# Performance work log

Hardware: AMD Instinct MI355X
Metric: run time of the kernel (lower is better)

The kernel has to match this reference:

```python
import jax, jax.numpy as jnp
import numpy as np

KERNEL = 3          # kernel_size = (3, 3)
DEGREE = 3          # spline_order -> Chebyshev polynomial degree
N_CONVS = 8


def setup_inputs() -> dict:
    key = jax.random.key(0)
    k1, k2, k3, k4 = jax.random.split(key, 4)
    x = jax.random.normal(k1, (16, 16, 128, 128), jnp.float32)
    # per-conv learned params of ChebyshevKANLinear(in=9, out=1), stacked over n_convs
    cheby_coeffs = jax.random.normal(k2, (N_CONVS, KERNEL * KERNEL, DEGREE + 1), jnp.float32) * 0.1
    base_weight = jax.random.normal(k3, (N_CONVS, KERNEL * KERNEL), jnp.float32) * (1.0 / 3.0)
    spline_scaler = 1.0 + 0.1 * jax.random.normal(k4, (N_CONVS, KERNEL * KERNEL), jnp.float32)
    return {"x": x, "cheby_coeffs": cheby_coeffs,
            "base_weight": base_weight, "spline_scaler": spline_scaler}


def _kan_conv2d(x, cheby_coeffs, base_weight, spline_scaler):
    # x: (B, C, H, W); each channel unfolded independently (as torch Unfold per-channel),
    # each of N_CONVS KAN kernels applied to every channel -> out channels C*N_CONVS.
    B, C, H, W = x.shape
    patches = jax.lax.conv_general_dilated_patches(
        x, (KERNEL, KERNEL), (1, 1), [(1, 1), (1, 1)])  # (B, C*9, Ho, Wo), channel-major
    Ho, Wo = patches.shape[-2], patches.shape[-1]
    p = patches.reshape(B, C, KERNEL * KERNEL, Ho * Wo)
    p = jnp.moveaxis(p, 2, 3)  # (B, C, P, 9) where P = Ho*Wo patches

    # base (skip) path: SiLU(x) @ base_weight^T
    base = jnp.einsum('bcpi,ji->bcjp', jax.nn.silu(p), base_weight)

    # spline path: Chebyshev basis on tanh-normalized input
    t = jnp.tanh(p)
    Ts = [jnp.ones_like(t), t]
    for _ in range(DEGREE - 1):
        Ts.append(2.0 * t * Ts[-1] - Ts[-2])
    Tb = jnp.stack(Ts, axis=-1)  # (B, C, P, 9, DEGREE+1)
    w = cheby_coeffs * spline_scaler[..., None]  # (n_convs, 9, D+1)
    spline = jnp.einsum('bcpik,jik->bcjp', Tb, w)

    out = (base + spline).reshape(B, C * N_CONVS, Ho, Wo)
    return out


def reference(x, cheby_coeffs, base_weight, spline_scaler):
    return _kan_conv2d(x, cheby_coeffs, base_weight, spline_scaler)
```

## Files before the change

### kernel.cpp

```cpp
#include <hip/hip_runtime.h>

#define BATCH 16
#define CH    16
#define HH    128
#define WW    128
#define NC    8
#define TR    8
#define HR    (TR + 2)
#define FW    (WW + 2)

__global__ __launch_bounds__(256, 4)
void kan_conv_kernel(const float* __restrict__ x,
                     const float* __restrict__ cheby,
                     const float* __restrict__ bwt,
                     const float* __restrict__ scl,
                     float* __restrict__ out)
{
    __shared__ float4 feat[HR][FW];
    __shared__ float4 wgt[9 * NC];
    __shared__ float  bias[NC];

    const int tid  = threadIdx.x;
    const int band = blockIdx.x * TR;
    const int bz   = blockIdx.y;

    if (tid < 9 * NC) {
        int j = tid / 9, i = tid % 9;
        float s = scl[j * 9 + i];
        wgt[i * NC + j] = make_float4(bwt[j * 9 + i],
                                      cheby[(j * 9 + i) * 4 + 1] * s,
                                      cheby[(j * 9 + i) * 4 + 2] * s,
                                      cheby[(j * 9 + i) * 4 + 3] * s);
    } else if (tid >= 128 && tid < 128 + NC) {
        int j = tid - 128;
        float b = 0.f;
        #pragma unroll
        for (int i = 0; i < 9; ++i)
            b += (cheby[(j * 9 + i) * 4 + 0] - cheby[(j * 9 + i) * 4 + 2]) * scl[j * 9 + i];
        bias[j] = b;
    }

    const float* xp = x + (size_t)bz * HH * WW;
    for (int idx = tid; idx < HR * FW; idx += 256) {
        int row = idx / FW;
        int col = idx - row * FW;
        int gh  = band + row - 1;
        int gw  = col - 1;
        float v = 0.f;
        if ((unsigned)gh < (unsigned)HH && (unsigned)gw < (unsigned)WW)
            v = xp[gh * WW + gw];
        float e1 = __expf(v);
        float e2 = e1 * e1;
        float sg = 1.f - __builtin_amdgcn_rcpf(1.f + e1);
        float t  = 1.f - 2.f * __builtin_amdgcn_rcpf(e2 + 1.f);
        float f2 = 2.f * t * t;
        float f3 = 2.f * t * (f2 - 1.f) - t;
        feat[row][col] = make_float4(v * sg, t, f2, f3);
    }
    __syncthreads();

    const int c  = tid & 127;
    const int r0 = tid >> 7;

    float acc[4][NC];
    #pragma unroll
    for (int s = 0; s < 4; ++s)
        #pragma unroll
        for (int j = 0; j < NC; ++j)
            acc[s][j] = bias[j];

    #pragma unroll
    for (int dr = 0; dr < 3; ++dr) {
        #pragma unroll
        for (int dc = 0; dc < 3; ++dc) {
            float4 f[4];
            #pragma unroll
            for (int s = 0; s < 4; ++s)
                f[s] = feat[r0 + 2 * s + dr][c + dc];
            #pragma unroll
            for (int j = 0; j < NC; ++j) {
                float4 w = wgt[(dr * 3 + dc) * NC + j];
                #pragma unroll
                for (int s = 0; s < 4; ++s) {
                    acc[s][j] += w.x * f[s].x;
                    acc[s][j] += w.y * f[s].y;
                    acc[s][j] += w.z * f[s].z;
                    acc[s][j] += w.w * f[s].w;
                }
            }
        }
    }

    float* op = out + (size_t)(bz * NC) * HH * WW + (size_t)(band + r0) * WW + c;
    #pragma unroll
    for (int j = 0; j < NC; ++j)
        #pragma unroll
        for (int s = 0; s < 4; ++s)
            op[(size_t)j * HH * WW + s * 2 * WW] = acc[s][j];
}

extern "C" void kernel_launch(void* const* d_in, const int* in_sizes, int n_in,
                              void* d_out, int out_size, void* d_ws, size_t ws_size,
                              hipStream_t stream) {
    const float* x     = (const float*)d_in[0];
    const float* cheby = (const float*)d_in[1];
    const float* bwt   = (const float*)d_in[2];
    const float* scl   = (const float*)d_in[3];
    float* out = (float*)d_out;

    dim3 grid(HH / TR, BATCH * CH);
    dim3 block(256);
    hipLaunchKernelGGL(kan_conv_kernel, grid, block, 0, stream, x, cheby, bwt, scl, out);
}
```

Measured before the change: 168.6 us.

## Pack output-channel pairs into v2f FMAs and reuse contiguous row features across taps

Each thread now computes 4 contiguous rows instead of 4 strided rows. It loads 6 feature rows per column offset once and reuses them across the 3 vertical taps, which cuts LDS reads. Weights are repacked as float2 pairs over output channels so the compiler can emit packed FMA (v_pk_fma_f32) and halve the FMA instruction count. Outputs are written with nontemporal stores to avoid polluting cache. The risks are higher register pressure from the 6 float4 features plus the v2f accumulators, and the stores are no longer perfectly interleaved across rows.

New measurement: 174.5 us. 3.5% more time.

```diff
diff --git a/kernel.cpp b/kernel.cpp
--- a/kernel.cpp
+++ b/kernel.cpp
@@ -8,6 +8,9 @@
 #define TR    8
 #define HR    (TR + 2)
 #define FW    (WW + 2)
+#define PLANE (HH * WW)
+
+typedef float v2f __attribute__((ext_vector_type(2)));
 
 __global__ __launch_bounds__(256, 4)
 void kan_conv_kernel(const float* __restrict__ x,
@@ -17,30 +20,38 @@
                      float* __restrict__ out)
 {
     __shared__ float4 feat[HR][FW];
-    __shared__ float4 wgt[9 * NC];
-    __shared__ float  bias[NC];
+    __shared__ v2f    wgt2[9][4][4];
+    __shared__ v2f    bias2[4];
 
     const int tid  = threadIdx.x;
     const int band = blockIdx.x * TR;
     const int bz   = blockIdx.y;
 
-    if (tid < 9 * NC) {
-        int j = tid / 9, i = tid % 9;
-        float s = scl[j * 9 + i];
-        wgt[i * NC + j] = make_float4(bwt[j * 9 + i],
-                                      cheby[(j * 9 + i) * 4 + 1] * s,
-                                      cheby[(j * 9 + i) * 4 + 2] * s,
-                                      cheby[(j * 9 + i) * 4 + 3] * s);
-    } else if (tid >= 128 && tid < 128 + NC) {
-        int j = tid - 128;
-        float b = 0.f;
+    if (tid < 9 * 4 * 4) {
+        int tap = tid >> 4, k = (tid >> 2) & 3, jp = tid & 3;
+        int j0 = jp * 2, j1 = j0 + 1;
+        v2f w;
+        if (k == 0) {
+            w.x = bwt[j0 * 9 + tap];
+            w.y = bwt[j1 * 9 + tap];
+        } else {
+            w.x = cheby[(j0 * 9 + tap) * 4 + k] * scl[j0 * 9 + tap];
+            w.y = cheby[(j1 * 9 + tap) * 4 + k] * scl[j1 * 9 + tap];
+        }
+        wgt2[tap][k][jp] = w;
+    } else if (tid >= 144 && tid < 148) {
+        int jp = tid - 144;
+        v2f b; b.x = 0.f; b.y = 0.f;
         #pragma unroll
-        for (int i = 0; i < 9; ++i)
-            b += (cheby[(j * 9 + i) * 4 + 0] - cheby[(j * 9 + i) * 4 + 2]) * scl[j * 9 + i];
-        bias[j] = b;
+        for (int i = 0; i < 9; ++i) {
+            int j0 = jp * 2, j1 = j0 + 1;
+            b.x += (cheby[(j0 * 9 + i) * 4 + 0] - cheby[(j0 * 9 + i) * 4 + 2]) * scl[j0 * 9 + i];
+            b.y += (cheby[(j1 * 9 + i) * 4 + 0] - cheby[(j1 * 9 + i) * 4 + 2]) * scl[j1 * 9 + i];
+        }
+        bias2[jp] = b;
     }
 
-    const float* xp = x + (size_t)bz * HH * WW;
+    const float* xp = x + (size_t)bz * PLANE;
     for (int idx = tid; idx < HR * FW; idx += 256) {
         int row = idx / FW;
         int col = idx - row * FW;
@@ -60,43 +71,50 @@
     __syncthreads();
 
     const int c  = tid & 127;
-    const int r0 = tid >> 7;
+    const int rb = (tid >> 7) * 4;
 
-    float acc[4][NC];
+    v2f acc[4][4];
     #pragma unroll
-    for (int s = 0; s < 4; ++s)
+    for (int r = 0; r < 4; ++r)
         #pragma unroll
-        for (int j = 0; j < NC; ++j)
-            acc[s][j] = bias[j];
+        for (int jp = 0; jp < 4; ++jp)
+            acc[r][jp] = bias2[jp];
 
     #pragma unroll
-    for (int dr = 0; dr < 3; ++dr) {
+    for (int dc = 0; dc < 3; ++dc) {
+        float4 f[6];
         #pragma unroll
-        for (int dc = 0; dc < 3; ++dc) {
-            float4 f[4];
+        for (int rr = 0; rr < 6; ++rr)
+            f[rr] = feat[rb + rr][c + dc];
+        #pragma unroll
+        for (int dr = 0; dr < 3; ++dr) {
+            const int tap = dr * 3 + dc;
             #pragma unroll
-            for (int s = 0; s < 4; ++s)
-                f[s] = feat[r0 + 2 * s + dr][c + dc];
-            #pragma unroll
-            for (int j = 0; j < NC; ++j) {
-                float4 w = wgt[(dr * 3 + dc) * NC + j];
+            for (int jp = 0; jp < 4; ++jp) {
+                v2f w0 = wgt2[tap][0][jp];
+                v2f w1 = wgt2[tap][1][jp];
+                v2f w2 = wgt2[tap][2][jp];
+                v2f w3 = wgt2[tap][3][jp];
                 #pragma unroll
-                for (int s = 0; s < 4; ++s) {
-                    acc[s][j] += w.x * f[s].x;
-                    acc[s][j] += w.y * f[s].y;
-                    acc[s][j] += w.z * f[s].z;
-                    acc[s][j] += w.w * f[s].w;
+                for (int r = 0; r < 4; ++r) {
+                    float4 fv = f[r + dr];
+                    acc[r][jp] += w0 * fv.x;
+                    acc[r][jp] += w1 * fv.y;
+                    acc[r][jp] += w2 * fv.z;
+                    acc[r][jp] += w3 * fv.w;
                 }
             }
         }
     }
 
-    float* op = out + (size_t)(bz * NC) * HH * WW + (size_t)(band + r0) * WW + c;
+    float* op = out + (size_t)(bz * NC) * PLANE + (size_t)(band + rb) * WW + c;
     #pragma unroll
-    for (int j = 0; j < NC; ++j)
+    for (int jp = 0; jp < 4; ++jp)
         #pragma unroll
-        for (int s = 0; s < 4; ++s)
-            op[(size_t)j * HH * WW + s * 2 * WW] = acc[s][j];
+        for (int r = 0; r < 4; ++r) {
+            __builtin_nontemporal_store(acc[r][jp].x, op + (size_t)(jp * 2)     * PLANE + r * WW);
+            __builtin_nontemporal_store(acc[r][jp].y, op + (size_t)(jp * 2 + 1) * PLANE + r * WW);
+        }
 }
 
 extern "C" void kernel_launch(void* const* d_in, const int* in_sizes, int n_in,
```
